# Optimization experiments

Hardware: AMD Instinct MI355X
Metric: run time of the kernel (lower is better)

Reference implementation:

```python
import jax, jax.numpy as jnp
import numpy as np

HIDDEN = 1024
HEADS = 16
HEAD_DIM = HIDDEN // HEADS


def setup_inputs() -> dict:
    key = jax.random.key(0)
    ks = jax.random.split(key, 11)
    s = 1.0 / np.sqrt(HIDDEN)
    return {
        "query": jax.random.normal(ks[0], (8, 1024, HIDDEN), dtype=jnp.float32),
        "key": jax.random.normal(ks[1], (8, 1024, HIDDEN), dtype=jnp.float32),
        "value": jax.random.normal(ks[2], (8, 1024, HIDDEN), dtype=jnp.float32),
        "Wq": jax.random.uniform(ks[3], (HIDDEN, HIDDEN), jnp.float32, -s, s),
        "bq": jax.random.uniform(ks[4], (HIDDEN,), jnp.float32, -s, s),
        "Wk": jax.random.uniform(ks[5], (HIDDEN, HIDDEN), jnp.float32, -s, s),
        "bk": jax.random.uniform(ks[6], (HIDDEN,), jnp.float32, -s, s),
        "Wv": jax.random.uniform(ks[7], (HIDDEN, HIDDEN), jnp.float32, -s, s),
        "bv": jax.random.uniform(ks[8], (HIDDEN,), jnp.float32, -s, s),
        "Wo": jax.random.uniform(ks[9], (HIDDEN, HIDDEN), jnp.float32, -s, s),
        "bo": jax.random.uniform(ks[10], (HIDDEN,), jnp.float32, -s, s),
    }


def reference(query, key, value, Wq, bq, Wk, bk, Wv, bv, Wo, bo):
    B, S, D = key.shape
    scale = jnp.sqrt(jnp.asarray(HEAD_DIM, dtype=query.dtype))
    # linear projections (torch Linear: x @ W.T + b), split into heads -> [B,H,S,hd]
    def proj(x, W, b):
        return (x @ W.T + b).reshape(B, -1, HEADS, HEAD_DIM).transpose(0, 2, 1, 3)
    q = proj(query, Wq, bq)
    k = proj(key, Wk, bk)
    v = proj(value, Wv, bv)
    # [B,H,Sq,Sk] full attention scores (module materializes them)
    energy = jnp.einsum("bhqd,bhkd->bhqk", q, k) / scale
    attention = jax.nn.softmax(energy, axis=-1)
    # dropout p=0.0 -> identity
    x = jnp.einsum("bhqk,bhkd->bhqd", attention, v)
    x = x.transpose(0, 2, 1, 3).reshape(B, -1, D)
    return x @ Wo.T + bo
```

## Files before the change

### kernel.cpp

```cpp
#include <hip/hip_runtime.h>
#include <hip/hip_bf16.h>
#include <stdint.h>

#define HIDDEN 1024
#define HEADS 16
#define HD 64
#define BATCH 8
#define SEQ 1024
#define MTOT (BATCH*SEQ)

typedef __attribute__((ext_vector_type(4))) float  f32x4;
typedef __attribute__((ext_vector_type(4))) float  float4v;
typedef __attribute__((ext_vector_type(8))) short  s16x8;
typedef __attribute__((ext_vector_type(4))) short  s16x4;
typedef __bf16 bf16x8 __attribute__((ext_vector_type(8)));

#define QSCALE 0.18033688011112042f

__device__ __forceinline__ short f2bf(float f) {
  uint32_t u = __builtin_bit_cast(uint32_t, f);
  u += 0x7FFFu + ((u >> 16) & 1u);
  return (short)(u >> 16);
}
__device__ __forceinline__ bf16x8 asbf(s16x8 v) {
  return __builtin_bit_cast(bf16x8, v);
}

__device__ __forceinline__ float dpp_fmax16(float x) {
  int t;
  t = __builtin_amdgcn_update_dpp(0, __builtin_bit_cast(int, x), 0xB1, 0xF, 0xF, true);
  x = fmaxf(x, __builtin_bit_cast(float, t));
  t = __builtin_amdgcn_update_dpp(0, __builtin_bit_cast(int, x), 0x4E, 0xF, 0xF, true);
  x = fmaxf(x, __builtin_bit_cast(float, t));
  t = __builtin_amdgcn_update_dpp(0, __builtin_bit_cast(int, x), 0x141, 0xF, 0xF, true);
  x = fmaxf(x, __builtin_bit_cast(float, t));
  t = __builtin_amdgcn_update_dpp(0, __builtin_bit_cast(int, x), 0x140, 0xF, 0xF, true);
  x = fmaxf(x, __builtin_bit_cast(float, t));
  return x;
}
__device__ __forceinline__ float dpp_fadd16(float x) {
  int t;
  t = __builtin_amdgcn_update_dpp(0, __builtin_bit_cast(int, x), 0xB1, 0xF, 0xF, true);
  x += __builtin_bit_cast(float, t);
  t = __builtin_amdgcn_update_dpp(0, __builtin_bit_cast(int, x), 0x4E, 0xF, 0xF, true);
  x += __builtin_bit_cast(float, t);
  t = __builtin_amdgcn_update_dpp(0, __builtin_bit_cast(int, x), 0x141, 0xF, 0xF, true);
  x += __builtin_bit_cast(float, t);
  t = __builtin_amdgcn_update_dpp(0, __builtin_bit_cast(int, x), 0x140, 0xF, 0xF, true);
  x += __builtin_bit_cast(float, t);
  return x;
}

typedef const __attribute__((address_space(1))) void* gvp;
typedef __attribute__((address_space(3)))       void* lvp;
__device__ __forceinline__ void gl_lds16(const void* g, const void* ldsbase) {
  __builtin_amdgcn_global_load_lds((gvp)(uintptr_t)g,
                                   (lvp)(uintptr_t)(uint32_t)(uintptr_t)ldsbase,
                                   16, 0, 0);
}

__global__ __launch_bounds__(256) void cvt_x(const float* __restrict__ src,
                                             short* __restrict__ dst) {
  int i = blockIdx.x * 256 + threadIdx.x;
  float4v a = *(const float4v*)(src + (size_t)i * 8);
  float4v b = *(const float4v*)(src + (size_t)i * 8 + 4);
  s16x8 o = { f2bf(a.x), f2bf(a.y), f2bf(a.z), f2bf(a.w),
              f2bf(b.x), f2bf(b.y), f2bf(b.z), f2bf(b.w) };
  *(s16x8*)(dst + (size_t)i * 8) = o;
}

__global__ __launch_bounds__(256) void cvt_w(const float* __restrict__ s0,
                                             const float* __restrict__ s1,
                                             const float* __restrict__ s2,
                                             const float* __restrict__ s3,
                                             short* __restrict__ dst) {
  int z = blockIdx.y;
  const float* src = (z == 0) ? s0 : (z == 1) ? s1 : (z == 2) ? s2 : s3;
  int i = blockIdx.x * 256 + threadIdx.x;
  float4v a = *(const float4v*)(src + (size_t)i * 8);
  float4v b = *(const float4v*)(src + (size_t)i * 8 + 4);
  s16x8 o = { f2bf(a.x), f2bf(a.y), f2bf(a.z), f2bf(a.w),
              f2bf(b.x), f2bf(b.y), f2bf(b.z), f2bf(b.w) };
  *(s16x8*)(dst + (size_t)z * 1048576 + (size_t)i * 8) = o;
}

__global__ __launch_bounds__(256) void vtrans(const short* __restrict__ Vb,
                                              short* __restrict__ Vt) {
  __shared__ short lt[64 * 64];
  const int t = threadIdx.x;
  const int kt0 = blockIdx.x, h = blockIdx.y, b = blockIdx.z;
  const short* src = Vb + ((size_t)(b * 1024 + kt0 * 64)) * 1024 + h * 64;

  #pragma unroll
  for (int i = 0; i < 2; i++) {
    int c = t + i * 256;
    int s = c >> 3, dc = c & 7;
    s16x8 v = *(const s16x8*)(src + (size_t)s * 1024 + dc * 8);
    int dcp = dc ^ (s & 7) ^ ((s >> 3) & 7);
    *(s16x8*)(&lt[s * 64 + dcp * 8]) = v;
  }
  __syncthreads();

  short* dst = Vt + ((size_t)(b * 16 + h) * 64) * 1024 + kt0 * 64;
  #pragma unroll
  for (int i = 0; i < 2; i++) {
    int c = t + i * 256;
    int d = c >> 3, kc = c & 7;
    s16x8 o;
    #pragma unroll
    for (int j = 0; j < 8; j++) {
      int s = kc * 8 + j;
      o[j] = lt[s * 64 + (((d >> 3) ^ j ^ kc) * 8) + (d & 7)];
    }
    *(s16x8*)(dst + (size_t)d * 1024 + (kc ^ (d & 7)) * 8) = o;
  }
}

template<int CMODE>
__global__ __launch_bounds__(256, 2) void gemm_bf16_dma(
    const short* __restrict__ A, const short* __restrict__ Wb,
    const float* __restrict__ bias, void* __restrict__ Cv, float scale)
{
  __shared__ short Alds[128 * 32];
  __shared__ short Blds[128 * 32];

  const int t  = threadIdx.x;
  const int w  = t >> 6, l = t & 63, g = l >> 4, ln = l & 15;
  const int wr = w >> 1, wc = w & 1;
  const int m0 = blockIdx.x * 128, n0 = blockIdx.y * 128;

  f32x4 acc[4][4];
  #pragma unroll
  for (int i = 0; i < 4; i++)
    #pragma unroll
    for (int j = 0; j < 4; j++) acc[i][j] = (f32x4)0.0f;

  for (int k0 = 0; k0 < 1024; k0 += 32) {
    #pragma unroll
    for (int i = 0; i < 2; i++) {
      int c = i * 256 + w * 64 + l;
      int row = c >> 2, col8 = c & 3;
      gl_lds16(A  + (size_t)(m0 + row) * 1024 + k0 + col8 * 8,
               &Alds[(i * 256 + w * 64) * 8]);
      gl_lds16(Wb + (size_t)(n0 + row) * 1024 + k0 + col8 * 8,
               &Blds[(i * 256 + w * 64) * 8]);
    }
    __syncthreads();

    s16x8 af[4], bfr[4];
    #pragma unroll
    for (int mf = 0; mf < 4; mf++)
      af[mf] = *(const s16x8*)(&Alds[(wr * 64 + mf * 16 + ln) * 32 + g * 8]);
    #pragma unroll
    for (int nf = 0; nf < 4; nf++)
      bfr[nf] = *(const s16x8*)(&Blds[(wc * 64 + nf * 16 + ln) * 32 + g * 8]);

    __builtin_amdgcn_s_setprio(1);
    #pragma unroll
    for (int mf = 0; mf < 4; mf++)
      #pragma unroll
      for (int nf = 0; nf < 4; nf++)
        acc[mf][nf] = __builtin_amdgcn_mfma_f32_16x16x32_bf16(
            asbf(af[mf]), asbf(bfr[nf]), acc[mf][nf], 0, 0, 0);
    __builtin_amdgcn_s_setprio(0);
    __syncthreads();
  }

  float bv[4];
  #pragma unroll
  for (int nf = 0; nf < 4; nf++) bv[nf] = bias[n0 + wc * 64 + nf * 16 + ln];
  #pragma unroll
  for (int mf = 0; mf < 4; mf++)
    #pragma unroll
    for (int nf = 0; nf < 4; nf++)
      #pragma unroll
      for (int r = 0; r < 4; r++) {
        float vv = (acc[mf][nf][r] + bv[nf]) * scale;
        size_t idx = (size_t)(m0 + wr * 64 + mf * 16 + g * 4 + r) * 1024
                   + n0 + wc * 64 + nf * 16 + ln;
        if constexpr (CMODE == 0) ((float*)Cv)[idx] = vv;
        else if constexpr (CMODE == 1) ((short*)Cv)[idx] = f2bf(vv);
        else {
          size_t idxs = idx ^ (size_t)(((g * 4 + r) & 7) * 8);
          ((short*)Cv)[idxs] = f2bf(vv);
        }
      }
}

template<bool A_IS_BF16, bool OUT_IS_F32>
__global__ __launch_bounds__(256, 2) void gemm_bt_bias(
    const void* __restrict__ Av, const float* __restrict__ W,
    const float* __restrict__ bias, void* __restrict__ Cv, float scale)
{
  __shared__ short Alds[128 * 32];
  __shared__ short Blds[128 * 32];

  const int t  = threadIdx.x;
  const int w  = t >> 6, l = t & 63, g = l >> 4, ln = l & 15;
  const int wr = w >> 1, wc = w & 1;
  const int m0 = blockIdx.x * 128, n0 = blockIdx.y * 128;

  f32x4 acc[4][4];
  #pragma unroll
  for (int i = 0; i < 4; i++)
    #pragma unroll
    for (int j = 0; j < 4; j++) acc[i][j] = (f32x4)0.0f;

  const float* Af = (const float*)Av;
  const short* Ab = (const short*)Av;

  for (int k0 = 0; k0 < 1024; k0 += 32) {
    if constexpr (!A_IS_BF16) {
      #pragma unroll
      for (int i = 0; i < 4; i++) {
        int c = i * 256 + t;
        int row = c >> 3, c4 = c & 7;
        float4v v = *(const float4v*)(Af + (size_t)(m0 + row) * 1024 + k0 + c4 * 4);
        s16x4 p = { f2bf(v.x), f2bf(v.y), f2bf(v.z), f2bf(v.w) };
        *(s16x4*)(&Alds[row * 32 + c4 * 4]) = p;
      }
    } else {
      #pragma unroll
      for (int i = 0; i < 2; i++) {
        int c = i * 256 + t;
        int row = c >> 2, c8 = c & 3;
        *(s16x8*)(&Alds[row * 32 + c8 * 8]) =
            *(const s16x8*)(Ab + (size_t)(m0 + row) * 1024 + k0 + c8 * 8);
      }
    }
    #pragma unroll
    for (int i = 0; i < 4; i++) {
      int c = i * 256 + t;
      int row = c >> 3, c4 = c & 7;
      float4v v = *(const float4v*)(W + (size_t)(n0 + row) * 1024 + k0 + c4 * 4);
      s16x4 p = { f2bf(v.x), f2bf(v.y), f2bf(v.z), f2bf(v.w) };
      *(s16x4*)(&Blds[row * 32 + c4 * 4]) = p;
    }
    __syncthreads();

    s16x8 af[4], bfr[4];
    #pragma unroll
    for (int mf = 0; mf < 4; mf++)
      af[mf] = *(const s16x8*)(&Alds[(wr * 64 + mf * 16 + ln) * 32 + g * 8]);
    #pragma unroll
    for (int nf = 0; nf < 4; nf++)
      bfr[nf] = *(const s16x8*)(&Blds[(wc * 64 + nf * 16 + ln) * 32 + g * 8]);

    #pragma unroll
    for (int mf = 0; mf < 4; mf++)
      #pragma unroll
      for (int nf = 0; nf < 4; nf++)
        acc[mf][nf] = __builtin_amdgcn_mfma_f32_16x16x32_bf16(
            asbf(af[mf]), asbf(bfr[nf]), acc[mf][nf], 0, 0, 0);
    __syncthreads();
  }

  float bv[4];
  #pragma unroll
  for (int nf = 0; nf < 4; nf++) bv[nf] = bias[n0 + wc * 64 + nf * 16 + ln];
  #pragma unroll
  for (int mf = 0; mf < 4; mf++)
    #pragma unroll
    for (int nf = 0; nf < 4; nf++)
      #pragma unroll
      for (int r = 0; r < 4; r++) {
        float vv = (acc[mf][nf][r] + bv[nf]) * scale;
        size_t idx = (size_t)(m0 + wr * 64 + mf * 16 + g * 4 + r) * 1024
                   + n0 + wc * 64 + nf * 16 + ln;
        if constexpr (OUT_IS_F32) ((float*)Cv)[idx] = vv;
        else                      ((short*)Cv)[idx] = f2bf(vv);
      }
}

__global__ __launch_bounds__(256, 2) void flash_attn(
    const short* __restrict__ Q, const short* __restrict__ Kswz,
    const short* __restrict__ Vt, short* __restrict__ CTX)
{
  __shared__ short Klds[2][64 * 64];
  __shared__ short Vlds[2][64 * 64];
  __shared__ short Plds[4][32 * 72];

  const int t  = threadIdx.x;
  const int w  = t >> 6, l = t & 63, g = l >> 4, ln = l & 15;
  const int bh   = blockIdx.x & 127;
  const int tile = blockIdx.x >> 7;
  const int b = bh >> 4, h = bh & 15;
  const size_t rowbase = (size_t)b * SEQ;
  const int colbase = h * HD;
  const int q0w = tile * 128 + w * 32;

  const short* Kg = Kswz + rowbase * 1024 + colbase;
  const short* Vg = Vt + (size_t)bh * 65536;
  const int c0 = w * 64 + l;

  s16x8 qf[2][2];
  #pragma unroll
  for (int mf = 0; mf < 2; mf++)
    #pragma unroll
    for (int kf = 0; kf < 2; kf++)
      qf[mf][kf] = *(const s16x8*)(Q + (rowbase + q0w + mf * 16 + ln) * 1024
                                     + colbase + kf * 32 + g * 8);

  f32x4 acc_o[2][4];
  #pragma unroll
  for (int i = 0; i < 2; i++)
    #pragma unroll
    for (int j = 0; j < 4; j++) acc_o[i][j] = (f32x4)0.0f;

  float m_run[2][4], l_run[2][4];
  #pragma unroll
  for (int i = 0; i < 2; i++)
    #pragma unroll
    for (int r = 0; r < 4; r++) { m_run[i][r] = -1e30f; l_run[i][r] = 0.0f; }

  auto STAGE = [&](int buf, int nt) {
    #pragma unroll
    for (int i = 0; i < 2; i++) {
      int c = c0 + i * 256;
      gl_lds16(Kg + (size_t)(nt * 64 + (c >> 3)) * 1024 + (c & 7) * 8,
               &Klds[buf][(i * 256 + w * 64) * 8]);
      gl_lds16(Vg + (size_t)(c >> 3) * 1024 + nt * 64 + (c & 7) * 8,
               &Vlds[buf][(i * 256 + w * 64) * 8]);
    }
  };

  STAGE(0, 0);
  __syncthreads();

  int cur = 0;
  for (int kt = 0; kt < 16; kt++) {
    if (kt < 15) STAGE(cur ^ 1, kt + 1);

    const short* Kc = &Klds[cur][0];
    const short* Vc = &Vlds[cur][0];

    f32x4 s_acc[2][4];
    #pragma unroll
    for (int i = 0; i < 2; i++)
      #pragma unroll
      for (int j = 0; j < 4; j++) s_acc[i][j] = (f32x4)0.0f;

    __builtin_amdgcn_s_setprio(1);
    #pragma unroll
    for (int kf = 0; kf < 2; kf++) {
      s16x8 kfr[4];
      #pragma unroll
      for (int nf = 0; nf < 4; nf++)
        kfr[nf] = *(const s16x8*)(Kc + (nf * 16 + ln) * 64
                                     + (((kf * 4 + g) ^ (ln & 7)) * 8));
      #pragma unroll
      for (int mf = 0; mf < 2; mf++)
        #pragma unroll
        for (int nf = 0; nf < 4; nf++)
          s_acc[mf][nf] = __builtin_amdgcn_mfma_f32_16x16x32_bf16(
              asbf(qf[mf][kf]), asbf(kfr[nf]), s_acc[mf][nf], 0, 0, 0);
    }
    __builtin_amdgcn_s_setprio(0);

    float tm = s_acc[0][0][0];
    #pragma unroll
    for (int mf = 0; mf < 2; mf++)
      #pragma unroll
      for (int nf = 0; nf < 4; nf++)
        #pragma unroll
        for (int r = 0; r < 4; r++) tm = fmaxf(tm, s_acc[mf][nf][r]);
    tm = dpp_fmax16(tm);
    tm = fmaxf(tm, __shfl_xor(tm, 16));
    tm = fmaxf(tm, __shfl_xor(tm, 32));
    float mn = m_run[0][0];
    #pragma unroll
    for (int mf = 0; mf < 2; mf++)
      #pragma unroll
      for (int r = 0; r < 4; r++) mn = fminf(mn, m_run[mf][r]);

    if (__all(tm - mn <= 8.0f)) {
      #pragma unroll
      for (int mf = 0; mf < 2; mf++)
        #pragma unroll
        for (int r = 0; r < 4; r++) {
          float m0v = m_run[mf][r];
          float rs = 0.0f;
          #pragma unroll
          for (int nf = 0; nf < 4; nf++) {
            float pv = exp2f(s_acc[mf][nf][r] - m0v);
            s_acc[mf][nf][r] = pv;
            rs += pv;
          }
          l_run[mf][r] += rs;
        }
    } else {
      #pragma unroll
      for (int mf = 0; mf < 2; mf++)
        #pragma unroll
        for (int r = 0; r < 4; r++) {
          float mx = fmaxf(fmaxf(s_acc[mf][0][r], s_acc[mf][1][r]),
                           fmaxf(s_acc[mf][2][r], s_acc[mf][3][r]));
          mx = dpp_fmax16(mx);
          float mnew = fmaxf(m_run[mf][r], mx);
          float sc = exp2f(m_run[mf][r] - mnew);
          m_run[mf][r] = mnew;
          float rs = 0.0f;
          #pragma unroll
          for (int nf = 0; nf < 4; nf++) {
            float pv = exp2f(s_acc[mf][nf][r] - mnew);
            s_acc[mf][nf][r] = pv;
            rs += pv;
          }
          l_run[mf][r] = l_run[mf][r] * sc + rs;
          #pragma unroll
          for (int nf = 0; nf < 4; nf++) acc_o[mf][nf][r] *= sc;
        }
    }

    short* Pw = &Plds[w][0];
    #pragma unroll
    for (int mf = 0; mf < 2; mf++)
      #pragma unroll
      for (int nf = 0; nf < 4; nf++) {
        uint32_t p01, p23;
        asm("v_cvt_pk_bf16_f32 %0, %1, %2"
            : "=v"(p01) : "v"(s_acc[mf][nf][0]), "v"(s_acc[mf][nf][1]));
        asm("v_cvt_pk_bf16_f32 %0, %1, %2"
            : "=v"(p23) : "v"(s_acc[mf][nf][2]), "v"(s_acc[mf][nf][3]));
        int pb = (mf * 16 + g * 4) * 72 + ((nf * 16 + ln) ^ (g << 3));
        Pw[pb]       = (short)p01;
        Pw[pb + 72]  = (short)(p01 >> 16);
        Pw[pb + 144] = (short)p23;
        Pw[pb + 216] = (short)(p23 >> 16);
      }

    s16x8 pa[2][2], vbf[4][2];
    #pragma unroll
    for (int mf = 0; mf < 2; mf++)
      #pragma unroll
      for (int kf = 0; kf < 2; kf++)
        pa[mf][kf] = *(const s16x8*)(
            &Pw[(mf * 16 + ln) * 72 + (((kf * 4 + g) ^ (ln >> 2)) << 3)]);
    #pragma unroll
    for (int nf = 0; nf < 4; nf++)
      #pragma unroll
      for (int kf = 0; kf < 2; kf++)
        vbf[nf][kf] = *(const s16x8*)(Vc + (nf * 16 + ln) * 64
                                         + (((kf * 4 + g) ^ (ln & 7)) * 8));

    __builtin_amdgcn_s_setprio(1);
    #pragma unroll
    for (int kf = 0; kf < 2; kf++)
      #pragma unroll
      for (int mf = 0; mf < 2; mf++)
        #pragma unroll
        for (int nf = 0; nf < 4; nf++)
          acc_o[mf][nf] = __builtin_amdgcn_mfma_f32_16x16x32_bf16(
              asbf(pa[mf][kf]), asbf(vbf[nf][kf]), acc_o[mf][nf], 0, 0, 0);
    __builtin_amdgcn_s_setprio(0);

    __syncthreads();
    cur ^= 1;
  }

  #pragma unroll
  for (int mf = 0; mf < 2; mf++)
    #pragma unroll
    for (int r = 0; r < 4; r++) {
      float inv = 1.0f / dpp_fadd16(l_run[mf][r]);
      size_t row = rowbase + q0w + mf * 16 + g * 4 + r;
      #pragma unroll
      for (int nf = 0; nf < 4; nf++)
        CTX[row * 1024 + colbase + nf * 16 + ln] = f2bf(acc_o[mf][nf][r] * inv);
    }
}

__global__ __launch_bounds__(256, 2) void flash_attn_fb(
    const short* __restrict__ Q, const short* __restrict__ K,
    const short* __restrict__ V, short* __restrict__ CTX)
{
  __shared__ short Klds[2][64 * 64];
  __shared__ short Vtl [2][64 * 64];
  __shared__ short Plds[4][32 * 72];

  const int t  = threadIdx.x;
  const int w  = t >> 6, l = t & 63, g = l >> 4, ln = l & 15;
  const int tile = blockIdx.x & 7;
  const int bh   = blockIdx.x >> 3;
  const int b = bh >> 4, h = bh & 15;
  const size_t rowbase = (size_t)b * SEQ;
  const int colbase = h * HD;
  const int q0w = tile * 128 + w * 32;

  const int kk0  = t >> 3;
  const int dblk = t & 7;
  const int ksw  = (dblk ^ (kk0 & 7)) * 8;
  const int kWr  = kk0 * 64 + dblk * 8;
  const short* Kg = K + rowbase * 1024 + colbase + ksw;
  const short* Vg = V + rowbase * 1024 + colbase + dblk * 8;

  s16x8 qf[2][2];
  #pragma unroll
  for (int mf = 0; mf < 2; mf++)
    #pragma unroll
    for (int kf = 0; kf < 2; kf++)
      qf[mf][kf] = *(const s16x8*)(Q + (rowbase + q0w + mf * 16 + ln) * 1024
                                     + colbase + kf * 32 + g * 8);

  f32x4 acc_o[2][4];
  #pragma unroll
  for (int i = 0; i < 2; i++)
    #pragma unroll
    for (int j = 0; j < 4; j++) acc_o[i][j] = (f32x4)0.0f;

  float m_run[2][4], l_run[2][4];
  #pragma unroll
  for (int i = 0; i < 2; i++)
    #pragma unroll
    for (int r = 0; r < 4; r++) { m_run[i][r] = -1e30f; l_run[i][r] = 0.0f; }

  auto storeKV = [&](int buf, s16x8 ka, s16x8 kb, s16x8 va, s16x8 vb8) {
    short* Kd = &Klds[buf][0];
    short* Vd = &Vtl[buf][0];
    *(s16x8*)(Kd + kWr)        = ka;
    *(s16x8*)(Kd + kWr + 2048) = kb;
    #pragma unroll
    for (int e = 0; e < 8; e++) {
      int a0 = (dblk * 8 + e) * 64 + (kk0 ^ ((e ^ dblk) * 8));
      Vd[a0]      = va[e];
      Vd[a0 ^ 32] = vb8[e];
    }
  };

  s16x8 kvA = *(const s16x8*)(Kg + (size_t)kk0 * 1024);
  s16x8 kvB = *(const s16x8*)(Kg + (size_t)(kk0 + 32) * 1024);
  s16x8 vvA = *(const s16x8*)(Vg + (size_t)kk0 * 1024);
  s16x8 vvB = *(const s16x8*)(Vg + (size_t)(kk0 + 32) * 1024);
  storeKV(0, kvA, kvB, vvA, vvB);

  int cur = 0;
  for (int kt = 0; kt < 16; kt++) {
    if (kt < 15) {
      const size_t r0 = (size_t)((kt + 1) * 64 + kk0) * 1024;
      kvA = *(const s16x8*)(Kg + r0);
      kvB = *(const s16x8*)(Kg + r0 + 32 * 1024);
      vvA = *(const s16x8*)(Vg + r0);
      vvB = *(const s16x8*)(Vg + r0 + 32 * 1024);
    }
    __syncthreads();

    const short* Kc = &Klds[cur][0];
    const short* Vc = &Vtl[cur][0];

    f32x4 s_acc[2][4];
    #pragma unroll
    for (int i = 0; i < 2; i++)
      #pragma unroll
      for (int j = 0; j < 4; j++) s_acc[i][j] = (f32x4)0.0f;

    #pragma unroll
    for (int kf = 0; kf < 2; kf++) {
      s16x8 kfr[4];
      #pragma unroll
      for (int nf = 0; nf < 4; nf++)
        kfr[nf] = *(const s16x8*)(Kc + (nf * 16 + ln) * 64
                                     + (((kf * 4 + g) ^ (ln & 7)) * 8));
      #pragma unroll
      for (int mf = 0; mf < 2; mf++)
        #pragma unroll
        for (int nf = 0; nf < 4; nf++)
          s_acc[mf][nf] = __builtin_amdgcn_mfma_f32_16x16x32_bf16(
              asbf(qf[mf][kf]), asbf(kfr[nf]), s_acc[mf][nf], 0, 0, 0);
    }

    float smax[2][4];
    float worst = -1e30f;
    #pragma unroll
    for (int mf = 0; mf < 2; mf++)
      #pragma unroll
      for (int r = 0; r < 4; r++) {
        float mx = fmaxf(fmaxf(s_acc[mf][0][r], s_acc[mf][1][r]),
                         fmaxf(s_acc[mf][2][r], s_acc[mf][3][r]));
        mx = dpp_fmax16(mx);
        smax[mf][r] = mx;
        worst = fmaxf(worst, mx - m_run[mf][r]);
      }

    if (__all(worst <= 8.0f)) {
      #pragma unroll
      for (int mf = 0; mf < 2; mf++)
        #pragma unroll
        for (int r = 0; r < 4; r++) {
          float m0v = m_run[mf][r];
          float rs = 0.0f;
          #pragma unroll
          for (int nf = 0; nf < 4; nf++) {
            float pv = exp2f(s_acc[mf][nf][r] - m0v);
            s_acc[mf][nf][r] = pv;
            rs += pv;
          }
          l_run[mf][r] += rs;
        }
    } else {
      #pragma unroll
      for (int mf = 0; mf < 2; mf++)
        #pragma unroll
        for (int r = 0; r < 4; r++) {
          float mnew = fmaxf(m_run[mf][r], smax[mf][r]);
          float sc = exp2f(m_run[mf][r] - mnew);
          m_run[mf][r] = mnew;
          float rs = 0.0f;
          #pragma unroll
          for (int nf = 0; nf < 4; nf++) {
            float pv = exp2f(s_acc[mf][nf][r] - mnew);
            s_acc[mf][nf][r] = pv;
            rs += pv;
          }
          l_run[mf][r] = l_run[mf][r] * sc + rs;
          #pragma unroll
          for (int nf = 0; nf < 4; nf++) acc_o[mf][nf][r] *= sc;
        }
    }

    short* Pw = &Plds[w][0];
    #pragma unroll
    for (int mf = 0; mf < 2; mf++)
      #pragma unroll
      for (int nf = 0; nf < 4; nf++) {
        uint32_t p01, p23;
        asm("v_cvt_pk_bf16_f32 %0, %1, %2"
            : "=v"(p01) : "v"(s_acc[mf][nf][0]), "v"(s_acc[mf][nf][1]));
        asm("v_cvt_pk_bf16_f32 %0, %1, %2"
            : "=v"(p23) : "v"(s_acc[mf][nf][2]), "v"(s_acc[mf][nf][3]));
        int pb = (mf * 16 + g * 4) * 72 + ((nf * 16 + ln) ^ (g << 3));
        Pw[pb]       = (short)p01;
        Pw[pb + 72]  = (short)(p01 >> 16);
        Pw[pb + 144] = (short)p23;
        Pw[pb + 216] = (short)(p23 >> 16);
      }

    s16x8 pa[2][2], vbf[4][2];
    #pragma unroll
    for (int mf = 0; mf < 2; mf++)
      #pragma unroll
      for (int kf = 0; kf < 2; kf++)
        pa[mf][kf] = *(const s16x8*)(
            &Pw[(mf * 16 + ln) * 72 + (((kf * 4 + g) ^ (ln >> 2)) << 3)]);
    #pragma unroll
    for (int nf = 0; nf < 4; nf++)
      #pragma unroll
      for (int kf = 0; kf < 2; kf++) {
        int d  = nf * 16 + ln;
        int sw = (d & 7) ^ (d >> 3);
        vbf[nf][kf] = *(const s16x8*)(Vc + d * 64 + ((kf * 32 + g * 8) ^ (sw * 8)));
      }

    #pragma unroll
    for (int kf = 0; kf < 2; kf++)
      #pragma unroll
      for (int mf = 0; mf < 2; mf++)
        #pragma unroll
        for (int nf = 0; nf < 4; nf++)
          acc_o[mf][nf] = __builtin_amdgcn_mfma_f32_16x16x32_bf16(
              asbf(pa[mf][kf]), asbf(vbf[nf][kf]), acc_o[mf][nf], 0, 0, 0);

    if (kt < 15) {
      storeKV(cur ^ 1, kvA, kvB, vvA, vvB);
      cur ^= 1;
    }
  }

  #pragma unroll
  for (int mf = 0; mf < 2; mf++)
    #pragma unroll
    for (int r = 0; r < 4; r++) {
      float inv = 1.0f / dpp_fadd16(l_run[mf][r]);
      size_t row = rowbase + q0w + mf * 16 + g * 4 + r;
      #pragma unroll
      for (int nf = 0; nf < 4; nf++)
        CTX[row * 1024 + colbase + nf * 16 + ln] = f2bf(acc_o[mf][nf][r] * inv);
    }
}

extern "C" void kernel_launch(void* const* d_in, const int* in_sizes, int n_in,
                              void* d_out, int out_size, void* d_ws, size_t ws_size,
                              hipStream_t stream) {
  const float* query = (const float*)d_in[0];
  const float* key   = (const float*)d_in[1];
  const float* value = (const float*)d_in[2];
  const float* Wq = (const float*)d_in[3];
  const float* bq = (const float*)d_in[4];
  const float* Wk = (const float*)d_in[5];
  const float* bk = (const float*)d_in[6];
  const float* Wv = (const float*)d_in[7];
  const float* bv = (const float*)d_in[8];
  const float* Wo = (const float*)d_in[9];
  const float* bo = (const float*)d_in[10];

  const size_t E = (size_t)MTOT * 1024;
  short* Qb = (short*)d_ws;
  short* Kb = Qb + E;
  short* Vb = Kb + E;
  short* Cx = Vb + E;
  short* T  = Cx + E;
  short* Wb = T  + E;

  const size_t need = (5 * E + 4ull * 1048576) * 2;
  dim3 gg(MTOT / 128, HIDDEN / 128), bb(256);
  dim3 fg(BATCH * HEADS * (SEQ / 128));

  if (ws_size >= need) {
    cvt_w<<<dim3(512, 4), bb, 0, stream>>>(Wq, Wk, Wv, Wo, Wb);
    cvt_x<<<4096, bb, 0, stream>>>(query, T);
    gemm_bf16_dma<1><<<gg, bb, 0, stream>>>(T, Wb + 0 * 1048576, bq, Qb, QSCALE);
    cvt_x<<<4096, bb, 0, stream>>>(key, T);
    gemm_bf16_dma<2><<<gg, bb, 0, stream>>>(T, Wb + 1 * 1048576, bk, Kb, 1.0f);
    cvt_x<<<4096, bb, 0, stream>>>(value, T);
    gemm_bf16_dma<1><<<gg, bb, 0, stream>>>(T, Wb + 2 * 1048576, bv, Vb, 1.0f);
    vtrans<<<dim3(16, 16, 8), bb, 0, stream>>>(Vb, T);
    flash_attn<<<fg, bb, 0, stream>>>(Qb, Kb, T, Cx);
    gemm_bf16_dma<0><<<gg, bb, 0, stream>>>(Cx, Wb + 3 * 1048576, bo, (float*)d_out, 1.0f);
  } else {
    gemm_bt_bias<false, false><<<gg, bb, 0, stream>>>(query, Wq, bq, Qb, QSCALE);
    gemm_bt_bias<false, false><<<gg, bb, 0, stream>>>(key,   Wk, bk, Kb, 1.0f);
    gemm_bt_bias<false, false><<<gg, bb, 0, stream>>>(value, Wv, bv, Vb, 1.0f);
    flash_attn_fb<<<fg, bb, 0, stream>>>(Qb, Kb, Vb, Cx);
    gemm_bt_bias<true, true><<<gg, bb, 0, stream>>>(Cx, Wo, bo, (float*)d_out, 1.0f);
  }
}
```

Measured before the change: 226.1 us.

## Compute transposed scores in flash attention and shuffle P through registers instead of LDS

The QK^T MFMA is swapped to produce S^T, so each lane holds one query column and the row max and sum need only two cross-lane shuffles instead of DPP reductions per row. The P matrix is repacked into the A-operand layout for the PV MFMA with lane permutes (shfl_xor 16/32) rather than a round trip through LDS. This removes the per-warp P buffer, which cuts LDS use, and launch bounds are raised from 2 to 4 blocks per SM. The cost is extra shuffles, including a per-row broadcast of the rescale factor and the final normaliser, plus added register pressure under the tighter launch bound.

```diff
diff --git a/kernel.cpp b/kernel.cpp
--- a/kernel.cpp
+++ b/kernel.cpp
@@ -13,6 +13,7 @@
 typedef __attribute__((ext_vector_type(4))) float  float4v;
 typedef __attribute__((ext_vector_type(8))) short  s16x8;
 typedef __attribute__((ext_vector_type(4))) short  s16x4;
+typedef __attribute__((ext_vector_type(4))) unsigned int u32x4;
 typedef __bf16 bf16x8 __attribute__((ext_vector_type(8)));
 
 #define QSCALE 0.18033688011112042f
@@ -272,16 +273,17 @@
       }
 }
 
-__global__ __launch_bounds__(256, 2) void flash_attn(
+__global__ __launch_bounds__(256, 4) void flash_attn(
     const short* __restrict__ Q, const short* __restrict__ Kswz,
     const short* __restrict__ Vt, short* __restrict__ CTX)
 {
   __shared__ short Klds[2][64 * 64];
   __shared__ short Vlds[2][64 * 64];
-  __shared__ short Plds[4][32 * 72];
 
   const int t  = threadIdx.x;
   const int w  = t >> 6, l = t & 63, g = l >> 4, ln = l & 15;
+  const int rb0 = g & 1, rb1 = g >> 1;
+  const bool sendK = (rb0 ^ rb1) != 0;
   const int bh   = blockIdx.x & 127;
   const int tile = blockIdx.x >> 7;
   const int b = bh >> 4, h = bh & 15;
@@ -307,11 +309,8 @@
     #pragma unroll
     for (int j = 0; j < 4; j++) acc_o[i][j] = (f32x4)0.0f;
 
-  float m_run[2][4], l_run[2][4];
-  #pragma unroll
-  for (int i = 0; i < 2; i++)
-    #pragma unroll
-    for (int r = 0; r < 4; r++) { m_run[i][r] = -1e30f; l_run[i][r] = 0.0f; }
+  float m_run[2] = { -1e30f, -1e30f };
+  float l_run[2] = { 0.0f, 0.0f };
 
   auto STAGE = [&](int buf, int nt) {
     #pragma unroll
@@ -334,11 +333,11 @@
     const short* Kc = &Klds[cur][0];
     const short* Vc = &Vlds[cur][0];
 
-    f32x4 s_acc[2][4];
-    #pragma unroll
-    for (int i = 0; i < 2; i++)
-      #pragma unroll
-      for (int j = 0; j < 4; j++) s_acc[i][j] = (f32x4)0.0f;
+    f32x4 sT[4][2];
+    #pragma unroll
+    for (int i = 0; i < 4; i++)
+      #pragma unroll
+      for (int j = 0; j < 2; j++) sT[i][j] = (f32x4)0.0f;
 
     __builtin_amdgcn_s_setprio(1);
     #pragma unroll
@@ -349,93 +348,104 @@
         kfr[nf] = *(const s16x8*)(Kc + (nf * 16 + ln) * 64
                                      + (((kf * 4 + g) ^ (ln & 7)) * 8));
       #pragma unroll
-      for (int mf = 0; mf < 2; mf++)
-        #pragma unroll
-        for (int nf = 0; nf < 4; nf++)
-          s_acc[mf][nf] = __builtin_amdgcn_mfma_f32_16x16x32_bf16(
-              asbf(qf[mf][kf]), asbf(kfr[nf]), s_acc[mf][nf], 0, 0, 0);
+      for (int kk4 = 0; kk4 < 4; kk4++)
+        #pragma unroll
+        for (int kq = 0; kq < 2; kq++)
+          sT[kk4][kq] = __builtin_amdgcn_mfma_f32_16x16x32_bf16(
+              asbf(kfr[kk4]), asbf(qf[kq][kf]), sT[kk4][kq], 0, 0, 0);
     }
     __builtin_amdgcn_s_setprio(0);
 
-    float tm = s_acc[0][0][0];
-    #pragma unroll
-    for (int mf = 0; mf < 2; mf++)
-      #pragma unroll
-      for (int nf = 0; nf < 4; nf++)
-        #pragma unroll
-        for (int r = 0; r < 4; r++) tm = fmaxf(tm, s_acc[mf][nf][r]);
-    tm = dpp_fmax16(tm);
-    tm = fmaxf(tm, __shfl_xor(tm, 16));
-    tm = fmaxf(tm, __shfl_xor(tm, 32));
-    float mn = m_run[0][0];
-    #pragma unroll
-    for (int mf = 0; mf < 2; mf++)
-      #pragma unroll
-      for (int r = 0; r < 4; r++) mn = fminf(mn, m_run[mf][r]);
-
-    if (__all(tm - mn <= 8.0f)) {
-      #pragma unroll
-      for (int mf = 0; mf < 2; mf++)
-        #pragma unroll
-        for (int r = 0; r < 4; r++) {
-          float m0v = m_run[mf][r];
-          float rs = 0.0f;
+    float rm[2];
+    #pragma unroll
+    for (int kq = 0; kq < 2; kq++) {
+      float mx = sT[0][kq][0];
+      #pragma unroll
+      for (int kk4 = 0; kk4 < 4; kk4++)
+        #pragma unroll
+        for (int r = 0; r < 4; r++)
+          if (kk4 | r) mx = fmaxf(mx, sT[kk4][kq][r]);
+      mx = fmaxf(mx, __shfl_xor(mx, 16));
+      mx = fmaxf(mx, __shfl_xor(mx, 32));
+      rm[kq] = mx;
+    }
+    float worst = fmaxf(rm[0] - m_run[0], rm[1] - m_run[1]);
+
+    if (__all(worst <= 8.0f)) {
+      #pragma unroll
+      for (int kq = 0; kq < 2; kq++) {
+        float m0v = m_run[kq];
+        float rs = 0.0f;
+        #pragma unroll
+        for (int kk4 = 0; kk4 < 4; kk4++)
           #pragma unroll
-          for (int nf = 0; nf < 4; nf++) {
-            float pv = exp2f(s_acc[mf][nf][r] - m0v);
-            s_acc[mf][nf][r] = pv;
+          for (int r = 0; r < 4; r++) {
+            float pv = exp2f(sT[kk4][kq][r] - m0v);
+            sT[kk4][kq][r] = pv;
             rs += pv;
           }
-          l_run[mf][r] += rs;
-        }
+        l_run[kq] += rs;
+      }
     } else {
-      #pragma unroll
-      for (int mf = 0; mf < 2; mf++)
-        #pragma unroll
-        for (int r = 0; r < 4; r++) {
-          float mx = fmaxf(fmaxf(s_acc[mf][0][r], s_acc[mf][1][r]),
-                           fmaxf(s_acc[mf][2][r], s_acc[mf][3][r]));
-          mx = dpp_fmax16(mx);
-          float mnew = fmaxf(m_run[mf][r], mx);
-          float sc = exp2f(m_run[mf][r] - mnew);
-          m_run[mf][r] = mnew;
-          float rs = 0.0f;
+      float sc[2];
+      #pragma unroll
+      for (int kq = 0; kq < 2; kq++) {
+        float mnew = fmaxf(m_run[kq], rm[kq]);
+        sc[kq] = exp2f(m_run[kq] - mnew);
+        m_run[kq] = mnew;
+        float rs = 0.0f;
+        #pragma unroll
+        for (int kk4 = 0; kk4 < 4; kk4++)
           #pragma unroll
-          for (int nf = 0; nf < 4; nf++) {
-            float pv = exp2f(s_acc[mf][nf][r] - mnew);
-            s_acc[mf][nf][r] = pv;
+          for (int r = 0; r < 4; r++) {
+            float pv = exp2f(sT[kk4][kq][r] - mnew);
+            sT[kk4][kq][r] = pv;
             rs += pv;
           }
-          l_run[mf][r] = l_run[mf][r] * sc + rs;
+        l_run[kq] = l_run[kq] * sc[kq] + rs;
+      }
+      #pragma unroll
+      for (int mf = 0; mf < 2; mf++)
+        #pragma unroll
+        for (int r = 0; r < 4; r++) {
+          float scr = __shfl(sc[mf], g * 4 + r);
           #pragma unroll
-          for (int nf = 0; nf < 4; nf++) acc_o[mf][nf][r] *= sc;
+          for (int nf = 0; nf < 4; nf++) acc_o[mf][nf][r] *= scr;
         }
     }
 
-    short* Pw = &Plds[w][0];
-    #pragma unroll
-    for (int mf = 0; mf < 2; mf++)
-      #pragma unroll
-      for (int nf = 0; nf < 4; nf++) {
-        uint32_t p01, p23;
+    uint32_t D[4][2][2];
+    #pragma unroll
+    for (int kk4 = 0; kk4 < 4; kk4++)
+      #pragma unroll
+      for (int kq = 0; kq < 2; kq++) {
         asm("v_cvt_pk_bf16_f32 %0, %1, %2"
-            : "=v"(p01) : "v"(s_acc[mf][nf][0]), "v"(s_acc[mf][nf][1]));
+            : "=v"(D[kk4][kq][0]) : "v"(sT[kk4][kq][0]), "v"(sT[kk4][kq][1]));
         asm("v_cvt_pk_bf16_f32 %0, %1, %2"
-            : "=v"(p23) : "v"(s_acc[mf][nf][2]), "v"(s_acc[mf][nf][3]));
-        int pb = (mf * 16 + g * 4) * 72 + ((nf * 16 + ln) ^ (g << 3));
-        Pw[pb]       = (short)p01;
-        Pw[pb + 72]  = (short)(p01 >> 16);
-        Pw[pb + 144] = (short)p23;
-        Pw[pb + 216] = (short)(p23 >> 16);
-      }
-
-    s16x8 pa[2][2], vbf[4][2];
-    #pragma unroll
-    for (int mf = 0; mf < 2; mf++)
-      #pragma unroll
-      for (int kf = 0; kf < 2; kf++)
-        pa[mf][kf] = *(const s16x8*)(
-            &Pw[(mf * 16 + ln) * 72 + (((kf * 4 + g) ^ (ln >> 2)) << 3)]);
+            : "=v"(D[kk4][kq][1]) : "v"(sT[kk4][kq][2]), "v"(sT[kk4][kq][3]));
+      }
+
+    s16x8 pa[2][2];
+    #pragma unroll
+    for (int kq = 0; kq < 2; kq++)
+      #pragma unroll
+      for (int kp = 0; kp < 2; kp++) {
+        uint32_t K0 = rb1 ? D[2*kp+1][kq][0] : D[2*kp][kq][0];
+        uint32_t K1 = rb1 ? D[2*kp+1][kq][1] : D[2*kp][kq][1];
+        uint32_t S0 = rb1 ? D[2*kp][kq][0]   : D[2*kp+1][kq][0];
+        uint32_t S1 = rb1 ? D[2*kp][kq][1]   : D[2*kp+1][kq][1];
+        uint32_t R0 = (uint32_t)__shfl_xor((int)S0, 32);
+        uint32_t R1 = (uint32_t)__shfl_xor((int)S1, 32);
+        uint32_t T0 = sendK ? K0 : R0, T1 = sendK ? K1 : R1;
+        uint32_t V0 = sendK ? R0 : K0, V1 = sendK ? R1 : K1;
+        uint32_t U0 = (uint32_t)__shfl_xor((int)T0, 16);
+        uint32_t U1 = (uint32_t)__shfl_xor((int)T1, 16);
+        u32x4 dw = { rb0 ? U0 : V0, rb0 ? U1 : V1,
+                     rb0 ? V0 : U0, rb0 ? V1 : U1 };
+        pa[kq][kp] = __builtin_bit_cast(s16x8, dw);
+      }
+
+    s16x8 vbf[4][2];
     #pragma unroll
     for (int nf = 0; nf < 4; nf++)
       #pragma unroll
@@ -459,10 +469,15 @@
   }
 
   #pragma unroll
+  for (int kq = 0; kq < 2; kq++) {
+    l_run[kq] += __shfl_xor(l_run[kq], 16);
+    l_run[kq] += __shfl_xor(l_run[kq], 32);
+  }
+  #pragma unroll
   for (int mf = 0; mf < 2; mf++)
     #pragma unroll
     for (int r = 0; r < 4; r++) {
-      float inv = 1.0f / dpp_fadd16(l_run[mf][r]);
+      float inv = 1.0f / __shfl(l_run[mf], g * 4 + r);
       size_t row = rowbase + q0w + mf * 16 + g * 4 + r;
       #pragma unroll
       for (int nf = 0; nf < 4; nf++)
```

Measured after the change: 359.1 us. 1.59x slower.
